# Optimization experiments

Hardware: AMD Instinct MI355X
Metric: run time of the kernel (lower is better)

The kernel has to match this reference:

```python
import jax, jax.numpy as jnp
import numpy as np

K = 5  # filter_size (matches init_kwargs)


def _adaptive_pool_matrix(size: int, k: int) -> jnp.ndarray:
    """Row-stochastic [k, size] matrix replicating torch adaptive_avg_pool1d bins."""
    P = np.zeros((k, size), np.float32)
    for i in range(k):
        s = (i * size) // k
        e = -((-(i + 1) * size) // k)  # ceil((i+1)*size/k)
        P[i, s:e] = 1.0 / (e - s)
    return jnp.asarray(P)


def setup_inputs() -> dict:
    key = jax.random.key(0)
    k1, k2, k3 = jax.random.split(key, 3)
    B, Cin, Cout, H, W = 8, 32, 32, 256, 256
    x = jax.random.normal(k1, (B, Cin, H, W), jnp.float32)
    conv_w = jax.random.normal(k2, (Cout, Cin), jnp.float32) * (1.0 / np.sqrt(Cin))
    conv_b = jax.random.normal(k3, (Cout,), jnp.float32) * 0.01
    return {"x": x, "conv_w": conv_w, "conv_b": conv_b}


def reference(x, conv_w, conv_b):
    B, Cin, H, W = x.shape
    # 1x1 conv == channel-mixing einsum
    feat = jnp.einsum('bihw,oi->bohw', x, conv_w) + conv_b[None, :, None, None]
    C = feat.shape[1]
    # adaptive_avg_pool2d(feat, K) via static pooling matrices -> per-(b,c) KxK filter
    Ph = _adaptive_pool_matrix(H, K)
    Pw = _adaptive_pool_matrix(W, K)
    filt = jnp.einsum('kh,bchw,lw->bckl', Ph, feat, Pw)  # [B, C, K, K]
    # pad per original intent ('same' output), then grouped conv with groups=B*C
    pad = (K - 1) // 2
    if (K - 1) % 2 == 0:
        p = ((pad, pad), (pad, pad))
    else:
        p = ((pad + 1, pad), (pad + 1, pad))
    inp = feat.reshape(1, B * C, H, W)
    w = filt.reshape(B * C, 1, K, K)
    out = jax.lax.conv_general_dilated(
        inp, w, window_strides=(1, 1), padding=p,
        dimension_numbers=('NCHW', 'OIHW', 'NCHW'),
        feature_group_count=B * C)
    return out.reshape(B, C, H, W)
```

## Files before the change

### kernel.cpp

```cpp
#include <hip/hip_runtime.h>


#define CIN 32
#define COUT 32
#define HW 256
#define PLANE (HW * HW)
#define BATCH 8
#define KF 5
#define BIN 52

__global__ __launch_bounds__(256) void conv_kernel(const float* __restrict__ x,
                                                   const float* __restrict__ Wm,
                                                   const float* __restrict__ bias,
                                                   float* __restrict__ feat) {
    int blk = blockIdx.x;
    int b   = blk >> 8;
    int row = blk & 255;
    int t   = threadIdx.x;

    const float* xb = x + (size_t)b * CIN * PLANE + (size_t)row * HW + t;
    float*       fb = feat + (size_t)b * COUT * PLANE + (size_t)row * HW + t;

    float acc[COUT];
#pragma unroll
    for (int o = 0; o < COUT; ++o) acc[o] = bias[o];

#pragma unroll
    for (int i = 0; i < CIN; ++i) {
        float xv = xb[(size_t)i * PLANE];
#pragma unroll
        for (int o = 0; o < COUT; ++o)
            acc[o] += Wm[o * CIN + i] * xv;
    }

#pragma unroll
    for (int o = 0; o < COUT; ++o)
        fb[(size_t)o * PLANE] = acc[o];
}

__global__ __launch_bounds__(256) void pool_x_kernel(const float* __restrict__ x,
                                                     float* __restrict__ xpool) {
    int blk   = blockIdx.x;
    int s     = blk & 7;
    int plane = blk >> 3;
    int t     = threadIdx.x;
    int gy0   = s * 32;

    const float* xp = x + (size_t)plane * PLANE + (size_t)gy0 * HW + t;
    float acc[KF] = {0.f, 0.f, 0.f, 0.f, 0.f};
#pragma unroll
    for (int r = 0; r < 32; ++r) {
        float v  = xp[(size_t)r * HW];
        int   gy = gy0 + r;
#pragma unroll
        for (int k = 0; k < KF; ++k) {
            const int sk = (k * HW) / KF;
            if (gy >= sk && gy < sk + BIN) acc[k] += v;
        }
    }

    __shared__ float lds[KF][HW + 1];
#pragma unroll
    for (int k = 0; k < KF; ++k) lds[k][t] = acc[k];
    __syncthreads();

    if (t < KF * KF) {
        int kk = t / KF, ll = t - kk * KF;
        int sl = (ll * HW) / KF;
        float ssum = 0.f;
#pragma unroll 4
        for (int w = 0; w < BIN; ++w) ssum += lds[kk][sl + w];
        atomicAdd(&xpool[plane * 25 + t], ssum);
    }
}

#define RS 16
#define LROW 264
__global__ __launch_bounds__(256, 6) void dwconv_kernel(const float* __restrict__ feat,
                                                        const float* __restrict__ xpool,
                                                        const float* __restrict__ Wm,
                                                        const float* __restrict__ bias,
                                                        float* __restrict__ out) {
    int bo    = blockIdx.y;
    int b     = bo >> 5;
    int o     = bo & 31;
    int strip = blockIdx.x;
    int gy0   = strip * RS;
    int t     = threadIdx.x;

    __shared__ __align__(16) float s[(RS + 4) * LROW];
    __shared__ float sfilt[25];

    if (t < 25) {
        float acc = bias[o] * 2704.0f;
        const float* xp = xpool + (size_t)b * CIN * 25 + t;
#pragma unroll
        for (int i = 0; i < CIN; ++i) acc += Wm[o * CIN + i] * xp[i * 25];
        sfilt[t] = acc * (1.0f / 2704.0f);
    }
    if (t < (RS + 4) * 4) {
        int lr = t >> 2, e = t & 3;
        int ci = (e < 2) ? (2 + e) : (258 + e);
        s[lr * LROW + ci] = 0.f;
    }

    const float* fb = feat + (size_t)bo * PLANE;
#pragma unroll
    for (int j = 0; j < 5; ++j) {
        int idx = t + 256 * j;
        int lr  = idx >> 6;
        int cx  = (idx & 63) * 4;
        int gy  = gy0 - 2 + lr;
        float4 v = {0.f, 0.f, 0.f, 0.f};
        if ((unsigned)gy < (unsigned)HW) v = *(const float4*)(fb + (size_t)gy * HW + cx);
        *(float4*)(&s[lr * LROW + 4 + cx]) = v;
    }
    __syncthreads();

    float fw[25];
#pragma unroll
    for (int j = 0; j < 25; ++j) fw[j] = sfilt[j];

    int c = t;
    float w0[5], w1[5], w2[5], w3[5], w4[5];
#pragma unroll
    for (int j = 0; j < 5; ++j) {
        w0[j] = s[0 * LROW + 2 + c + j];
        w1[j] = s[1 * LROW + 2 + c + j];
        w2[j] = s[2 * LROW + 2 + c + j];
        w3[j] = s[3 * LROW + 2 + c + j];
    }
    float* ob = out + (size_t)bo * PLANE + (size_t)gy0 * HW + c;
#pragma unroll
    for (int r = 0; r < RS; ++r) {
#pragma unroll
        for (int j = 0; j < 5; ++j) w4[j] = s[(r + 4) * LROW + 2 + c + j];
        float acc = 0.f;
#pragma unroll
        for (int j = 0; j < 5; ++j) {
            acc += fw[0 * 5 + j] * w0[j];
            acc += fw[1 * 5 + j] * w1[j];
            acc += fw[2 * 5 + j] * w2[j];
            acc += fw[3 * 5 + j] * w3[j];
            acc += fw[4 * 5 + j] * w4[j];
        }
        ob[(size_t)r * HW] = acc;
#pragma unroll
        for (int j = 0; j < 5; ++j) {
            w0[j] = w1[j]; w1[j] = w2[j]; w2[j] = w3[j]; w3[j] = w4[j];
        }
    }
}

extern "C" void kernel_launch(void* const* d_in, const int* in_sizes, int n_in,
                              void* d_out, int out_size, void* d_ws, size_t ws_size,
                              hipStream_t stream) {
    const float* x      = (const float*)d_in[0];
    const float* conv_w = (const float*)d_in[1];
    const float* conv_b = (const float*)d_in[2];
    float* out = (float*)d_out;

    float* feat  = (float*)d_ws;
    float* xpool = feat + (size_t)BATCH * COUT * PLANE;

    hipMemsetAsync(xpool, 0, BATCH * CIN * 25 * sizeof(float), stream);
    conv_kernel<<<dim3(BATCH * 256), dim3(256), 0, stream>>>(x, conv_w, conv_b, feat);
    pool_x_kernel<<<dim3(2048), dim3(256), 0, stream>>>(x, xpool);
    dwconv_kernel<<<dim3(HW / RS, BATCH * COUT), dim3(256), 0, stream>>>(feat, xpool, conv_w, conv_b, out);
}
```

Measured before the change: 164.8 us.

## Fuse conv and pooling kernels; replace atomics with per-strip partial sums

Merges the 1x1 conv kernel and the input-pooling kernel into one launch, with odd blocks doing pooling and even blocks doing conv, interleaved. Pooling blocks now write per-strip partial sums instead of atomically adding, which removes the memset and the atomics. The dwconv kernel sums the 8 partials while building each filter. This saves one launch and the memset, and may let x reads be shared through cache, at the cost of a few extra loads in the filter setup and an LDS allocation on conv blocks.

After: 245.2 us. 1.49x slower.

```diff
diff --git a/kernel.cpp b/kernel.cpp
--- a/kernel.cpp
+++ b/kernel.cpp
@@ -9,75 +9,76 @@
 #define KF 5
 #define BIN 52
 
-__global__ __launch_bounds__(256) void conv_kernel(const float* __restrict__ x,
-                                                   const float* __restrict__ Wm,
-                                                   const float* __restrict__ bias,
-                                                   float* __restrict__ feat) {
+__global__ __launch_bounds__(256) void conv_pool_kernel(const float* __restrict__ x,
+                                                        const float* __restrict__ Wm,
+                                                        const float* __restrict__ bias,
+                                                        float* __restrict__ feat,
+                                                        float* __restrict__ xpool_part) {
     int blk = blockIdx.x;
-    int b   = blk >> 8;
-    int row = blk & 255;
     int t   = threadIdx.x;
 
-    const float* xb = x + (size_t)b * CIN * PLANE + (size_t)row * HW + t;
-    float*       fb = feat + (size_t)b * COUT * PLANE + (size_t)row * HW + t;
+    __shared__ float plds[KF][HW + 1];
 
-    float acc[COUT];
+    if (blk & 1) {
+        int pb    = blk >> 1;
+        int s     = pb & 7;
+        int plane = pb >> 3;
+        int gy0   = s * 32;
+
+        const float* xp = x + (size_t)plane * PLANE + (size_t)gy0 * HW + t;
+        float acc[KF] = {0.f, 0.f, 0.f, 0.f, 0.f};
 #pragma unroll
-    for (int o = 0; o < COUT; ++o) acc[o] = bias[o];
+        for (int r = 0; r < 32; ++r) {
+            float v  = xp[(size_t)r * HW];
+            int   gy = gy0 + r;
+#pragma unroll
+            for (int k = 0; k < KF; ++k) {
+                const int sk = (k * HW) / KF;
+                if (gy >= sk && gy < sk + BIN) acc[k] += v;
+            }
+        }
+#pragma unroll
+        for (int k = 0; k < KF; ++k) plds[k][t] = acc[k];
+        __syncthreads();
+
+        if (t < KF * KF) {
+            int kk = t / KF, ll = t - kk * KF;
+            int sl = (ll * HW) / KF;
+            float ssum = 0.f;
+#pragma unroll 4
+            for (int w = 0; w < BIN; ++w) ssum += plds[kk][sl + w];
+            xpool_part[(size_t)plane * 200 + s * 25 + t] = ssum;
+        }
+    } else {
+        int cb  = blk >> 1;
+        int b   = cb >> 8;
+        int row = cb & 255;
+
+        const float* xb = x + (size_t)b * CIN * PLANE + (size_t)row * HW + t;
+        float*       fb = feat + (size_t)b * COUT * PLANE + (size_t)row * HW + t;
+
+        float acc[COUT];
+#pragma unroll
+        for (int o = 0; o < COUT; ++o) acc[o] = bias[o];
 
 #pragma unroll
-    for (int i = 0; i < CIN; ++i) {
-        float xv = xb[(size_t)i * PLANE];
+        for (int i = 0; i < CIN; ++i) {
+            float xv = xb[(size_t)i * PLANE];
+#pragma unroll
+            for (int o = 0; o < COUT; ++o)
+                acc[o] += Wm[o * CIN + i] * xv;
+        }
+
 #pragma unroll
         for (int o = 0; o < COUT; ++o)
-            acc[o] += Wm[o * CIN + i] * xv;
-    }
-
-#pragma unroll
-    for (int o = 0; o < COUT; ++o)
-        fb[(size_t)o * PLANE] = acc[o];
-}
-
-__global__ __launch_bounds__(256) void pool_x_kernel(const float* __restrict__ x,
-                                                     float* __restrict__ xpool) {
-    int blk   = blockIdx.x;
-    int s     = blk & 7;
-    int plane = blk >> 3;
-    int t     = threadIdx.x;
-    int gy0   = s * 32;
-
-    const float* xp = x + (size_t)plane * PLANE + (size_t)gy0 * HW + t;
-    float acc[KF] = {0.f, 0.f, 0.f, 0.f, 0.f};
-#pragma unroll
-    for (int r = 0; r < 32; ++r) {
-        float v  = xp[(size_t)r * HW];
-        int   gy = gy0 + r;
-#pragma unroll
-        for (int k = 0; k < KF; ++k) {
-            const int sk = (k * HW) / KF;
-            if (gy >= sk && gy < sk + BIN) acc[k] += v;
-        }
-    }
-
-    __shared__ float lds[KF][HW + 1];
-#pragma unroll
-    for (int k = 0; k < KF; ++k) lds[k][t] = acc[k];
-    __syncthreads();
-
-    if (t < KF * KF) {
-        int kk = t / KF, ll = t - kk * KF;
-        int sl = (ll * HW) / KF;
-        float ssum = 0.f;
-#pragma unroll 4
-        for (int w = 0; w < BIN; ++w) ssum += lds[kk][sl + w];
-        atomicAdd(&xpool[plane * 25 + t], ssum);
+            fb[(size_t)o * PLANE] = acc[o];
     }
 }
 
 #define RS 16
 #define LROW 264
 __global__ __launch_bounds__(256, 6) void dwconv_kernel(const float* __restrict__ feat,
-                                                        const float* __restrict__ xpool,
+                                                        const float* __restrict__ xpool_part,
                                                         const float* __restrict__ Wm,
                                                         const float* __restrict__ bias,
                                                         float* __restrict__ out) {
@@ -92,11 +93,17 @@
     __shared__ float sfilt[25];
 
     if (t < 25) {
-        float acc = bias[o] * 2704.0f;
-        const float* xp = xpool + (size_t)b * CIN * 25 + t;
+        float accf = bias[o] * 2704.0f;
+        const float* xp = xpool_part + (size_t)b * CIN * 200 + t;
 #pragma unroll
-        for (int i = 0; i < CIN; ++i) acc += Wm[o * CIN + i] * xp[i * 25];
-        sfilt[t] = acc * (1.0f / 2704.0f);
+        for (int i = 0; i < CIN; ++i) {
+            float w = Wm[o * CIN + i];
+            float p = 0.f;
+#pragma unroll
+            for (int s2 = 0; s2 < 8; ++s2) p += xp[i * 200 + s2 * 25];
+            accf += w * p;
+        }
+        sfilt[t] = accf * (1.0f / 2704.0f);
     }
     if (t < (RS + 4) * 4) {
         int lr = t >> 2, e = t & 3;
@@ -160,11 +167,9 @@
     const float* conv_b = (const float*)d_in[2];
     float* out = (float*)d_out;
 
-    float* feat  = (float*)d_ws;
-    float* xpool = feat + (size_t)BATCH * COUT * PLANE;
+    float* feat       = (float*)d_ws;
+    float* xpool_part = feat + (size_t)BATCH * COUT * PLANE;
 
-    hipMemsetAsync(xpool, 0, BATCH * CIN * 25 * sizeof(float), stream);
-    conv_kernel<<<dim3(BATCH * 256), dim3(256), 0, stream>>>(x, conv_w, conv_b, feat);
-    pool_x_kernel<<<dim3(2048), dim3(256), 0, stream>>>(x, xpool);
-    dwconv_kernel<<<dim3(HW / RS, BATCH * COUT), dim3(256), 0, stream>>>(feat, xpool, conv_w, conv_b, out);
+    conv_pool_kernel<<<dim3(4096), dim3(256), 0, stream>>>(x, conv_w, conv_b, feat, xpool_part);
+    dwconv_kernel<<<dim3(HW / RS, BATCH * COUT), dim3(256), 0, stream>>>(feat, xpool_part, conv_w, conv_b, out);
 }
```

## Merge conv and pool kernels; read feat directly in dwconv with taller strips

Applied to the files above, without the earlier changes.

The 1x1 conv kernel and the x-pooling kernel are combined into one launch, with block index deciding which path runs, so one kernel launch and its tail disappear. The depthwise conv kernel no longer stages a feat tile in shared memory. Each thread now reads its 5-wide row window straight from global memory, relying on cache for the horizontal overlap, and each strip grows from 16 to 32 rows. This removes the LDS staging and its barrier, but adds redundant global/L1 loads and boundary predicates.

Result: no change. 166.8 us (+1.2%).

```diff
diff --git a/kernel.cpp b/kernel.cpp
--- a/kernel.cpp
+++ b/kernel.cpp
@@ -9,111 +9,90 @@
 #define KF 5
 #define BIN 52
 
-__global__ __launch_bounds__(256) void conv_kernel(const float* __restrict__ x,
-                                                   const float* __restrict__ Wm,
-                                                   const float* __restrict__ bias,
-                                                   float* __restrict__ feat) {
+__global__ __launch_bounds__(256) void conv_pool_kernel(const float* __restrict__ x,
+                                                        const float* __restrict__ Wm,
+                                                        const float* __restrict__ bias,
+                                                        float* __restrict__ feat,
+                                                        float* __restrict__ xpool) {
     int blk = blockIdx.x;
-    int b   = blk >> 8;
-    int row = blk & 255;
     int t   = threadIdx.x;
 
-    const float* xb = x + (size_t)b * CIN * PLANE + (size_t)row * HW + t;
-    float*       fb = feat + (size_t)b * COUT * PLANE + (size_t)row * HW + t;
+    __shared__ float plds[KF][HW + 1];
 
-    float acc[COUT];
+    if (blk < 2048) {
+        int b   = blk >> 8;
+        int row = blk & 255;
+
+        const float* xb = x + (size_t)b * CIN * PLANE + (size_t)row * HW + t;
+        float*       fb = feat + (size_t)b * COUT * PLANE + (size_t)row * HW + t;
+
+        float acc[COUT];
 #pragma unroll
-    for (int o = 0; o < COUT; ++o) acc[o] = bias[o];
+        for (int o = 0; o < COUT; ++o) acc[o] = bias[o];
 
 #pragma unroll
-    for (int i = 0; i < CIN; ++i) {
-        float xv = xb[(size_t)i * PLANE];
+        for (int i = 0; i < CIN; ++i) {
+            float xv = xb[(size_t)i * PLANE];
+#pragma unroll
+            for (int o = 0; o < COUT; ++o)
+                acc[o] += Wm[o * CIN + i] * xv;
+        }
+
 #pragma unroll
         for (int o = 0; o < COUT; ++o)
-            acc[o] += Wm[o * CIN + i] * xv;
-    }
+            fb[(size_t)o * PLANE] = acc[o];
+    } else {
+        int pb    = blk - 2048;
+        int s     = pb & 7;
+        int plane = pb >> 3;
+        int gy0   = s * 32;
 
+        const float* xp = x + (size_t)plane * PLANE + (size_t)gy0 * HW + t;
+        float acc[KF] = {0.f, 0.f, 0.f, 0.f, 0.f};
 #pragma unroll
-    for (int o = 0; o < COUT; ++o)
-        fb[(size_t)o * PLANE] = acc[o];
-}
+        for (int r = 0; r < 32; ++r) {
+            float v  = xp[(size_t)r * HW];
+            int   gy = gy0 + r;
+#pragma unroll
+            for (int k = 0; k < KF; ++k) {
+                const int sk = (k * HW) / KF;
+                if (gy >= sk && gy < sk + BIN) acc[k] += v;
+            }
+        }
+#pragma unroll
+        for (int k = 0; k < KF; ++k) plds[k][t] = acc[k];
+        __syncthreads();
 
-__global__ __launch_bounds__(256) void pool_x_kernel(const float* __restrict__ x,
-                                                     float* __restrict__ xpool) {
-    int blk   = blockIdx.x;
-    int s     = blk & 7;
-    int plane = blk >> 3;
-    int t     = threadIdx.x;
-    int gy0   = s * 32;
-
-    const float* xp = x + (size_t)plane * PLANE + (size_t)gy0 * HW + t;
-    float acc[KF] = {0.f, 0.f, 0.f, 0.f, 0.f};
-#pragma unroll
-    for (int r = 0; r < 32; ++r) {
-        float v  = xp[(size_t)r * HW];
-        int   gy = gy0 + r;
-#pragma unroll
-        for (int k = 0; k < KF; ++k) {
-            const int sk = (k * HW) / KF;
-            if (gy >= sk && gy < sk + BIN) acc[k] += v;
+        if (t < KF * KF) {
+            int kk = t / KF, ll = t - kk * KF;
+            int sl = (ll * HW) / KF;
+            float ssum = 0.f;
+#pragma unroll 4
+            for (int w = 0; w < BIN; ++w) ssum += plds[kk][sl + w];
+            atomicAdd(&xpool[plane * 25 + t], ssum);
         }
-    }
-
-    __shared__ float lds[KF][HW + 1];
-#pragma unroll
-    for (int k = 0; k < KF; ++k) lds[k][t] = acc[k];
-    __syncthreads();
-
-    if (t < KF * KF) {
-        int kk = t / KF, ll = t - kk * KF;
-        int sl = (ll * HW) / KF;
-        float ssum = 0.f;
-#pragma unroll 4
-        for (int w = 0; w < BIN; ++w) ssum += lds[kk][sl + w];
-        atomicAdd(&xpool[plane * 25 + t], ssum);
     }
 }
 
-#define RS 16
-#define LROW 264
-__global__ __launch_bounds__(256, 6) void dwconv_kernel(const float* __restrict__ feat,
-                                                        const float* __restrict__ xpool,
-                                                        const float* __restrict__ Wm,
-                                                        const float* __restrict__ bias,
-                                                        float* __restrict__ out) {
+__global__ __launch_bounds__(256) void dwconv_kernel(const float* __restrict__ feat,
+                                                     const float* __restrict__ xpool,
+                                                     const float* __restrict__ Wm,
+                                                     const float* __restrict__ bias,
+                                                     float* __restrict__ out) {
     int bo    = blockIdx.y;
     int b     = bo >> 5;
     int o     = bo & 31;
     int strip = blockIdx.x;
-    int gy0   = strip * RS;
+    int gy0   = strip * 32;
     int t     = threadIdx.x;
 
-    __shared__ __align__(16) float s[(RS + 4) * LROW];
     __shared__ float sfilt[25];
-
     if (t < 25) {
-        float acc = bias[o] * 2704.0f;
+        float accf = bias[o] * 2704.0f;
         const float* xp = xpool + (size_t)b * CIN * 25 + t;
 #pragma unroll
-        for (int i = 0; i < CIN; ++i) acc += Wm[o * CIN + i] * xp[i * 25];
-        sfilt[t] = acc * (1.0f / 2704.0f);
-    }
-    if (t < (RS + 4) * 4) {
-        int lr = t >> 2, e = t & 3;
-        int ci = (e < 2) ? (2 + e) : (258 + e);
-        s[lr * LROW + ci] = 0.f;
-    }
-
-    const float* fb = feat + (size_t)bo * PLANE;
-#pragma unroll
-    for (int j = 0; j < 5; ++j) {
-        int idx = t + 256 * j;
-        int lr  = idx >> 6;
-        int cx  = (idx & 63) * 4;
-        int gy  = gy0 - 2 + lr;
-        float4 v = {0.f, 0.f, 0.f, 0.f};
-        if ((unsigned)gy < (unsigned)HW) v = *(const float4*)(fb + (size_t)gy * HW + cx);
-        *(float4*)(&s[lr * LROW + 4 + cx]) = v;
+        for (int i = 0; i < CIN; ++i) accf += Wm[o * CIN + i] * xp[i * 25];
+        sfilt[t] = accf * (1.0f / 2704.0f);
     }
     __syncthreads();
 
@@ -121,20 +100,33 @@
 #pragma unroll
     for (int j = 0; j < 25; ++j) fw[j] = sfilt[j];
 
+    const float* fb = feat + (size_t)bo * PLANE;
     int c = t;
+
+    bool cv[5];
+#pragma unroll
+    for (int j = 0; j < 5; ++j) cv[j] = (unsigned)(c + j - 2) < (unsigned)HW;
+
     float w0[5], w1[5], w2[5], w3[5], w4[5];
 #pragma unroll
     for (int j = 0; j < 5; ++j) {
-        w0[j] = s[0 * LROW + 2 + c + j];
-        w1[j] = s[1 * LROW + 2 + c + j];
-        w2[j] = s[2 * LROW + 2 + c + j];
-        w3[j] = s[3 * LROW + 2 + c + j];
+        int cc = c + j - 2;
+        w0[j] = (cv[j] && gy0 - 2 >= 0) ? fb[(size_t)(gy0 - 2) * HW + cc] : 0.f;
+        w1[j] = (cv[j] && gy0 - 1 >= 0) ? fb[(size_t)(gy0 - 1) * HW + cc] : 0.f;
+        w2[j] =  cv[j]                  ? fb[(size_t)(gy0    ) * HW + cc] : 0.f;
+        w3[j] =  cv[j]                  ? fb[(size_t)(gy0 + 1) * HW + cc] : 0.f;
     }
+
     float* ob = out + (size_t)bo * PLANE + (size_t)gy0 * HW + c;
 #pragma unroll
-    for (int r = 0; r < RS; ++r) {
+    for (int r = 0; r < 32; ++r) {
+        int  gy = gy0 + r + 2;
+        bool rv = gy < HW;
 #pragma unroll
-        for (int j = 0; j < 5; ++j) w4[j] = s[(r + 4) * LROW + 2 + c + j];
+        for (int j = 0; j < 5; ++j) {
+            int cc = c + j - 2;
+            w4[j] = (rv && cv[j]) ? fb[(size_t)gy * HW + cc] : 0.f;
+        }
         float acc = 0.f;
 #pragma unroll
         for (int j = 0; j < 5; ++j) {
@@ -164,7 +156,6 @@
     float* xpool = feat + (size_t)BATCH * COUT * PLANE;
 
     hipMemsetAsync(xpool, 0, BATCH * CIN * 25 * sizeof(float), stream);
-    conv_kernel<<<dim3(BATCH * 256), dim3(256), 0, stream>>>(x, conv_w, conv_b, feat);
-    pool_x_kernel<<<dim3(2048), dim3(256), 0, stream>>>(x, xpool);
-    dwconv_kernel<<<dim3(HW / RS, BATCH * COUT), dim3(256), 0, stream>>>(feat, xpool, conv_w, conv_b, out);
+    conv_pool_kernel<<<dim3(4096), dim3(256), 0, stream>>>(x, conv_w, conv_b, feat, xpool);
+    dwconv_kernel<<<dim3(8, BATCH * COUT), dim3(256), 0, stream>>>(feat, xpool, conv_w, conv_b, out);
 }
```
